# Kernel tuning notes

Measured on AMD Instinct MI355X. Metric: run time of the kernel, lower is better.

## Reference

```python
import jax, jax.numpy as jnp
import numpy as np

H = 1024   # hidden_size
V = 32000  # output_size (vocab)
S = 2048   # encoder seq_len


def setup_inputs() -> dict:
    key = jax.random.key(0)
    ks = jax.random.split(key, 12)
    s = 0.02
    return {
        "word_input": jax.random.randint(ks[0], (1,), 0, V),
        "last_hidden": jax.random.normal(ks[1], (1, 1, H), dtype=jnp.float32),
        "encoder_outputs": jax.random.normal(ks[2], (S, H), dtype=jnp.float32),
        "embedding": jax.random.normal(ks[3], (V, H), dtype=jnp.float32) * s,
        "attn_W": jax.random.normal(ks[4], (H, H), dtype=jnp.float32) * s,
        "attn_b": jax.random.normal(ks[5], (H,), dtype=jnp.float32) * s,
        "gru_W_ih": jax.random.normal(ks[6], (3 * H, 2 * H), dtype=jnp.float32) * s,
        "gru_W_hh": jax.random.normal(ks[7], (3 * H, H), dtype=jnp.float32) * s,
        "gru_b_ih": jax.random.normal(ks[8], (3 * H,), dtype=jnp.float32) * s,
        "gru_b_hh": jax.random.normal(ks[9], (3 * H,), dtype=jnp.float32) * s,
        "out_W": jax.random.normal(ks[10], (V, H), dtype=jnp.float32) * s,
        "out_b": jax.random.normal(ks[11], (V,), dtype=jnp.float32) * s,
    }


def reference(word_input, last_hidden, encoder_outputs, embedding,
              attn_W, attn_b, gru_W_ih, gru_W_hh, gru_b_ih, gru_b_hh,
              out_W, out_b):
    # embedding lookup; dropout is identity in eval mode
    word_embedded = embedding[word_input].reshape(1, 1, -1)  # [1,1,H]
    h = last_hidden[0, 0]  # [H]

    # vectorized version of the per-timestep loop: score_i = h . (W e_i + b)
    scores = (encoder_outputs @ attn_W.T + attn_b) @ h  # [S]
    # original applies softmax to each SCALAR -> all ones (zero grad), reproduce faithfully
    attn_weights = jax.nn.softmax(scores[:, None], axis=1)[:, 0]  # [S], == 1.0

    attn_applied = attn_weights @ encoder_outputs  # [H]
    rnn_input = jax.nn.relu(jnp.concatenate([word_embedded[0, 0], attn_applied]))  # [2H]

    # single-step GRU cell (PyTorch gate layout [r, z, n])
    gi = gru_W_ih @ rnn_input + gru_b_ih  # [3H]
    gh = gru_W_hh @ h + gru_b_hh          # [3H]
    i_r, i_z, i_n = jnp.split(gi, 3)
    h_r, h_z, h_n = jnp.split(gh, 3)
    r = jax.nn.sigmoid(i_r + h_r)
    z = jax.nn.sigmoid(i_z + h_z)
    n = jnp.tanh(i_n + r * h_n)
    h_new = (1.0 - z) * n + z * h  # [H]

    logits = h_new @ out_W.T + out_b  # [V]
    output = jax.nn.log_softmax(logits[None, :], axis=1)  # [1,V]
    return output, h_new.reshape(1, 1, H), attn_weights
```

## Files before the change

### kernel.cpp

```cpp
#include <hip/hip_runtime.h>


namespace {
constexpr int H = 1024;
constexpr int V = 32000;
constexpr int S = 2048;
constexpr int NTHR = 256;
constexpr int CS_BLKS = 32;
constexpr int CS_ROWS = S / CS_BLKS;
constexpr int GRU_BLKS = 768;
constexpr int D1_BLKS = CS_BLKS + GRU_BLKS + 1;
constexpr int D2_BLKS = 192;
constexpr int D3_BLKS = 1000;
constexpr int RPW = 8;
constexpr int D4_BLKS = V / NTHR;
}

__device__ __forceinline__ float wave_sum(float v) {
#pragma unroll
    for (int off = 32; off > 0; off >>= 1) v += __shfl_xor(v, off, 64);
    return v;
}
__device__ __forceinline__ float wave_max(float v) {
#pragma unroll
    for (int off = 32; off > 0; off >>= 1) v = fmaxf(v, __shfl_xor(v, off, 64));
    return v;
}
__device__ __forceinline__ float dot4(float4 a, float4 b) {
    return a.x * b.x + a.y * b.y + a.z * b.z + a.w * b.w;
}

__global__ __launch_bounds__(NTHR) void k_front(
    const float* __restrict__ enc, const float* __restrict__ Whh,
    const float* __restrict__ Wih, const float* __restrict__ bih,
    const float* __restrict__ bhh, const float* __restrict__ hin,
    const float* __restrict__ emb, const int* __restrict__ word,
    float* __restrict__ part, float* __restrict__ gi, float* __restrict__ gh,
    float* __restrict__ out) {
    const int b = blockIdx.x, t = threadIdx.x;
    if (b < CS_BLKS) {
        const float4* e = (const float4*)enc + (size_t)b * CS_ROWS * (H / 4) + t;
        float4 acc = make_float4(0.f, 0.f, 0.f, 0.f);
#pragma unroll
        for (int r = 0; r < CS_ROWS; ++r) {
            float4 v = e[(size_t)r * (H / 4)];
            acc.x += v.x; acc.y += v.y; acc.z += v.z; acc.w += v.w;
        }
        ((float4*)part)[b * (H / 4) + t] = acc;
    } else if (b < CS_BLKS + GRU_BLKS) {
        const int lane = t & 63, w = t >> 6;
        const int row = (b - CS_BLKS) * 4 + w;
        const float4* wh = (const float4*)Whh + (size_t)row * (H / 4);
        const float4* xh = (const float4*)hin;
        const float4* wi = (const float4*)Wih + (size_t)row * (2 * H / 4);
        const float4* er = (const float4*)emb + (size_t)word[0] * (H / 4);
        float ah = 0.f, ai = 0.f;
#pragma unroll
        for (int it = 0; it < 4; ++it) {
            const int idx = it * 64 + lane;
            ah += dot4(wh[idx], xh[idx]);
            float4 e4 = er[idx];
            e4.x = fmaxf(e4.x, 0.f); e4.y = fmaxf(e4.y, 0.f);
            e4.z = fmaxf(e4.z, 0.f); e4.w = fmaxf(e4.w, 0.f);
            ai += dot4(wi[idx], e4);
        }
        ah = wave_sum(ah);
        ai = wave_sum(ai);
        if (lane == 0) {
            gh[row] = ah + bhh[row];
            gi[row] = ai + bih[row];
        }
    } else {
#pragma unroll
        for (int k = 0; k < S / NTHR; ++k) out[V + H + k * NTHR + t] = 1.0f;
    }
}

__global__ __launch_bounds__(NTHR) void k_gi2(
    const float* __restrict__ Wih, const float* __restrict__ part,
    float* __restrict__ gi2) {
    __shared__ float4 rn[H / 4];
    const int t = threadIdx.x, lane = t & 63, w = t >> 6;
    float4 acc = make_float4(0.f, 0.f, 0.f, 0.f);
#pragma unroll
    for (int c = 0; c < CS_BLKS; ++c) {
        float4 v = ((const float4*)part)[c * (H / 4) + t];
        acc.x += v.x; acc.y += v.y; acc.z += v.z; acc.w += v.w;
    }
    acc.x = fmaxf(acc.x, 0.f); acc.y = fmaxf(acc.y, 0.f);
    acc.z = fmaxf(acc.z, 0.f); acc.w = fmaxf(acc.w, 0.f);
    rn[t] = acc;
    __syncthreads();
#pragma unroll
    for (int i = 0; i < 4; ++i) {
        const int row = blockIdx.x * 16 + w * 4 + i;
        const float4* wr = (const float4*)Wih + (size_t)row * (2 * H / 4) + (H / 4);
        float a = 0.f;
#pragma unroll
        for (int it = 0; it < 4; ++it) {
            const int idx = it * 64 + lane;
            a += dot4(wr[idx], rn[idx]);
        }
        a = wave_sum(a);
        if (lane == 0) gi2[row] = a;
    }
}

__global__ __launch_bounds__(NTHR) void k_logits(
    const float* __restrict__ gi, const float* __restrict__ gi2,
    const float* __restrict__ gh, const float* __restrict__ hin,
    const float* __restrict__ Wout, const float* __restrict__ bout,
    float* __restrict__ out, float* __restrict__ partm, float* __restrict__ parts) {
    __shared__ float hnew[H];
    __shared__ float bm[4], bs[4];
    const int t = threadIdx.x, lane = t & 63, w = t >> 6;
#pragma unroll
    for (int q = 0; q < 4; ++q) {
        const int j = q * NTHR + t;
        const float gr = gi[j] + gi2[j] + gh[j];
        const float gz = gi[H + j] + gi2[H + j] + gh[H + j];
        const float r = 1.f / (1.f + expf(-gr));
        const float z = 1.f / (1.f + expf(-gz));
        const float n = tanhf(gi[2 * H + j] + gi2[2 * H + j] + r * gh[2 * H + j]);
        const float hv = (1.f - z) * n + z * hin[j];
        hnew[j] = hv;
        if (blockIdx.x == 0) out[V + j] = hv;
    }
    __syncthreads();
    const float4* hn4 = (const float4*)hnew;
    const float4 x0 = hn4[lane], x1 = hn4[64 + lane];
    const float4 x2 = hn4[128 + lane], x3 = hn4[192 + lane];
    float a[RPW];
#pragma unroll 2
    for (int i = 0; i < RPW; ++i) {
        const int row = blockIdx.x * 32 + w * RPW + i;
        const float4* wr = (const float4*)Wout + (size_t)row * (H / 4);
        float v = dot4(wr[lane], x0) + dot4(wr[64 + lane], x1) +
                  dot4(wr[128 + lane], x2) + dot4(wr[192 + lane], x3);
        a[i] = wave_sum(v) + bout[row];
        if (lane == 0) out[row] = a[i];
    }
    float m = a[0];
#pragma unroll
    for (int i = 1; i < RPW; ++i) m = fmaxf(m, a[i]);
    float s = 0.f;
#pragma unroll
    for (int i = 0; i < RPW; ++i) s += expf(a[i] - m);
    if (lane == 0) { bm[w] = m; bs[w] = s; }
    __syncthreads();
    if (t == 0) {
        const float M = fmaxf(fmaxf(bm[0], bm[1]), fmaxf(bm[2], bm[3]));
        const float ss = bs[0] * expf(bm[0] - M) + bs[1] * expf(bm[1] - M) +
                         bs[2] * expf(bm[2] - M) + bs[3] * expf(bm[3] - M);
        partm[blockIdx.x] = M;
        parts[blockIdx.x] = ss;
    }
}

__global__ __launch_bounds__(NTHR) void k_final(
    const float* __restrict__ partm, const float* __restrict__ parts,
    float* __restrict__ out) {
    __shared__ float ms[4], ss[4];
    const int t = threadIdx.x, lane = t & 63, w = t >> 6;
    float m = -3.4e38f;
    for (int k = t; k < D3_BLKS; k += NTHR) m = fmaxf(m, partm[k]);
    m = wave_max(m);
    if (lane == 0) ms[w] = m;
    __syncthreads();
    const float M = fmaxf(fmaxf(ms[0], ms[1]), fmaxf(ms[2], ms[3]));
    float s = 0.f;
    for (int k = t; k < D3_BLKS; k += NTHR) s += parts[k] * expf(partm[k] - M);
    s = wave_sum(s);
    if (lane == 0) ss[w] = s;
    __syncthreads();
    const float L = logf(ss[0] + ss[1] + ss[2] + ss[3]);
    const int g = blockIdx.x * NTHR + t;
    out[g] = out[g] - M - L;
}

extern "C" void kernel_launch(void* const* d_in, const int* in_sizes, int n_in,
                              void* d_out, int out_size, void* d_ws, size_t ws_size,
                              hipStream_t stream) {
    const int*   word = (const int*)d_in[0];
    const float* hin  = (const float*)d_in[1];
    const float* enc  = (const float*)d_in[2];
    const float* emb  = (const float*)d_in[3];
    const float* Wih  = (const float*)d_in[6];
    const float* Whh  = (const float*)d_in[7];
    const float* bih  = (const float*)d_in[8];
    const float* bhh  = (const float*)d_in[9];
    const float* Wout = (const float*)d_in[10];
    const float* bout = (const float*)d_in[11];
    float* out = (float*)d_out;
    float* ws  = (float*)d_ws;

    float* part  = ws;
    float* gi    = part + CS_BLKS * H;
    float* gi2   = gi + 3 * H;
    float* gh    = gi2 + 3 * H;
    float* partm = gh + 3 * H;
    float* parts = partm + D3_BLKS;

    k_front<<<D1_BLKS, NTHR, 0, stream>>>(enc, Whh, Wih, bih, bhh, hin, emb, word,
                                          part, gi, gh, out);
    k_gi2<<<D2_BLKS, NTHR, 0, stream>>>(Wih, part, gi2);
    k_logits<<<D3_BLKS, NTHR, 0, stream>>>(gi, gi2, gh, hin, Wout, bout, out,
                                           partm, parts);
    k_final<<<D4_BLKS, NTHR, 0, stream>>>(partm, parts, out);
}
```

Baseline: 47.92 us.

## Finish column-sum reduction in last-arriving block and widen logits rows per block

Splits the encoder column sum across 128 blocks instead of 32. The last block to arrive, found with an atomic counter, reduces the partials and writes the ReLU'd attention vector once. Previously each of the 192 gi2 blocks re-reduced all partials itself. The logits kernel now handles 64 rows per block over 500 blocks with deeper unrolling. The counter is never reset and relies on modulo arithmetic across calls, and the extra fences and serialized final reduction add latency in the front kernel.

New measurement: 71.79 us. +49.8%, slower.

```diff
diff --git a/kernel.cpp b/kernel.cpp
--- a/kernel.cpp
+++ b/kernel.cpp
@@ -6,13 +6,13 @@
 constexpr int V = 32000;
 constexpr int S = 2048;
 constexpr int NTHR = 256;
-constexpr int CS_BLKS = 32;
+constexpr int CS_BLKS = 128;
 constexpr int CS_ROWS = S / CS_BLKS;
 constexpr int GRU_BLKS = 768;
 constexpr int D1_BLKS = CS_BLKS + GRU_BLKS + 1;
 constexpr int D2_BLKS = 192;
-constexpr int D3_BLKS = 1000;
-constexpr int RPW = 8;
+constexpr int D3_BLKS = 500;
+constexpr int RPW = 16;
 constexpr int D4_BLKS = V / NTHR;
 }
 
@@ -35,9 +35,11 @@
     const float* __restrict__ Wih, const float* __restrict__ bih,
     const float* __restrict__ bhh, const float* __restrict__ hin,
     const float* __restrict__ emb, const int* __restrict__ word,
-    float* __restrict__ part, float* __restrict__ gi, float* __restrict__ gh,
-    float* __restrict__ out) {
+    float* __restrict__ part, float* __restrict__ rn,
+    float* __restrict__ gi, float* __restrict__ gh,
+    float* __restrict__ out, int* __restrict__ ctrA) {
     const int b = blockIdx.x, t = threadIdx.x;
+    __shared__ int win;
     if (b < CS_BLKS) {
         const float4* e = (const float4*)enc + (size_t)b * CS_ROWS * (H / 4) + t;
         float4 acc = make_float4(0.f, 0.f, 0.f, 0.f);
@@ -47,6 +49,25 @@
             acc.x += v.x; acc.y += v.y; acc.z += v.z; acc.w += v.w;
         }
         ((float4*)part)[b * (H / 4) + t] = acc;
+        __threadfence();
+        __syncthreads();
+        if (t == 0) {
+            const int old = __hip_atomic_fetch_add(ctrA, 1, __ATOMIC_ACQ_REL,
+                                                   __HIP_MEMORY_SCOPE_AGENT);
+            win = ((old & (CS_BLKS - 1)) == CS_BLKS - 1);
+        }
+        __syncthreads();
+        if (win) {
+            __threadfence();
+            float4 s = make_float4(0.f, 0.f, 0.f, 0.f);
+            for (int c = 0; c < CS_BLKS; ++c) {
+                float4 v = ((const float4*)part)[c * (H / 4) + t];
+                s.x += v.x; s.y += v.y; s.z += v.z; s.w += v.w;
+            }
+            s.x = fmaxf(s.x, 0.f); s.y = fmaxf(s.y, 0.f);
+            s.z = fmaxf(s.z, 0.f); s.w = fmaxf(s.w, 0.f);
+            ((float4*)rn)[t] = s;
+        }
     } else if (b < CS_BLKS + GRU_BLKS) {
         const int lane = t & 63, w = t >> 6;
         const int row = (b - CS_BLKS) * 4 + w;
@@ -77,19 +98,11 @@
 }
 
 __global__ __launch_bounds__(NTHR) void k_gi2(
-    const float* __restrict__ Wih, const float* __restrict__ part,
+    const float* __restrict__ Wih, const float* __restrict__ rn,
     float* __restrict__ gi2) {
-    __shared__ float4 rn[H / 4];
+    __shared__ float4 sh[H / 4];
     const int t = threadIdx.x, lane = t & 63, w = t >> 6;
-    float4 acc = make_float4(0.f, 0.f, 0.f, 0.f);
-#pragma unroll
-    for (int c = 0; c < CS_BLKS; ++c) {
-        float4 v = ((const float4*)part)[c * (H / 4) + t];
-        acc.x += v.x; acc.y += v.y; acc.z += v.z; acc.w += v.w;
-    }
-    acc.x = fmaxf(acc.x, 0.f); acc.y = fmaxf(acc.y, 0.f);
-    acc.z = fmaxf(acc.z, 0.f); acc.w = fmaxf(acc.w, 0.f);
-    rn[t] = acc;
+    sh[t] = ((const float4*)rn)[t];
     __syncthreads();
 #pragma unroll
     for (int i = 0; i < 4; ++i) {
@@ -99,7 +112,7 @@
 #pragma unroll
         for (int it = 0; it < 4; ++it) {
             const int idx = it * 64 + lane;
-            a += dot4(wr[idx], rn[idx]);
+            a += dot4(wr[idx], sh[idx]);
         }
         a = wave_sum(a);
         if (lane == 0) gi2[row] = a;
@@ -131,9 +144,9 @@
     const float4 x0 = hn4[lane], x1 = hn4[64 + lane];
     const float4 x2 = hn4[128 + lane], x3 = hn4[192 + lane];
     float a[RPW];
-#pragma unroll 2
+#pragma unroll 4
     for (int i = 0; i < RPW; ++i) {
-        const int row = blockIdx.x * 32 + w * RPW + i;
+        const int row = blockIdx.x * 64 + w * RPW + i;
         const float4* wr = (const float4*)Wout + (size_t)row * (H / 4);
         float v = dot4(wr[lane], x0) + dot4(wr[64 + lane], x1) +
                   dot4(wr[128 + lane], x2) + dot4(wr[192 + lane], x3);
@@ -192,18 +205,20 @@
     const float* Wout = (const float*)d_in[10];
     const float* bout = (const float*)d_in[11];
     float* out = (float*)d_out;
-    float* ws  = (float*)d_ws;
-
+
+    int* ctrA = (int*)d_ws;
+    float* ws = (float*)d_ws + 64;
     float* part  = ws;
-    float* gi    = part + CS_BLKS * H;
+    float* rn    = part + CS_BLKS * H;
+    float* gi    = rn + H;
     float* gi2   = gi + 3 * H;
     float* gh    = gi2 + 3 * H;
     float* partm = gh + 3 * H;
     float* parts = partm + D3_BLKS;
 
     k_front<<<D1_BLKS, NTHR, 0, stream>>>(enc, Whh, Wih, bih, bhh, hin, emb, word,
-                                          part, gi, gh, out);
-    k_gi2<<<D2_BLKS, NTHR, 0, stream>>>(Wih, part, gi2);
+                                          part, rn, gi, gh, out, ctrA);
+    k_gi2<<<D2_BLKS, NTHR, 0, stream>>>(Wih, rn, gi2);
     k_logits<<<D3_BLKS, NTHR, 0, stream>>>(gi, gi2, gh, hin, Wout, bout, out,
                                            partm, parts);
     k_final<<<D4_BLKS, NTHR, 0, stream>>>(partm, parts, out);
```
